# Performance work log

Measured on AMD Instinct MI355X. Metric: run time of the kernel, lower is better.

The kernel has to match this reference:

```python
import jax, jax.numpy as jnp
import numpy as np

B, D, N = 8192, 1024, 4096     # batch, input_dim, num_outputs
SEG, W_SEG = 256, 16           # 256 uniform segments of width 16 (SEG*W_SEG == N)
TAU = 0.2                      # gumbel-softmax temperature


def setup_inputs() -> dict:
    key = jax.random.key(0)
    k1, k2, k3, k4 = jax.random.split(key, 4)
    bound = 1.0 / np.sqrt(D)   # init_bounded from the original module
    x = jax.random.normal(k1, (B, D), jnp.float32)
    W = jax.random.uniform(k2, (D, N), jnp.float32, -bound, bound)
    b = jax.random.uniform(k3, (N,), jnp.float32, -bound, bound)
    # Standard Gumbel(0,1) noise, precomputed for determinism: g = -log(-log(U))
    u = jax.random.uniform(k4, (B, N), jnp.float32, 1e-10, 1.0)
    gumbel = -jnp.log(-jnp.log(u))
    # segment flags: 0 -> tanh, nonzero -> gumbel-softmax (alternating)
    flags = (jnp.arange(SEG) % 2).astype(jnp.int32)
    return {"x": x, "W": W, "b": b, "gumbel": gumbel, "flags": flags}


def reference(x, W, b, gumbel, flags):
    # Dense layer
    outputs = x @ W + b                        # [B, N]
    # Segments are uniform-width, so the per-segment slice loop collapses to a reshape.
    y = outputs.reshape(B, SEG, W_SEG)         # [B, SEG, W_SEG]
    g = gumbel.reshape(B, SEG, W_SEG)
    # gumbel-softmax over each segment (hard=False path of the original)
    soft = jax.nn.softmax((y + g) / TAU, axis=-1)
    # per-segment dispatch: flag==0 -> tanh, else gumbel-softmax
    data_t = jnp.where(flags[None, :, None] == 0, jnp.tanh(y), soft)
    return outputs, data_t.reshape(B, N)
```

## Files before the change

kernel.cpp:

```cpp
#include <hip/hip_runtime.h>
#include <hip/hip_bf16.h>

#define B_DIM 8192
#define D_DIM 1024
#define N_DIM 4096
#define TAU_INV 5.0f

typedef __bf16 bf16x8 __attribute__((ext_vector_type(8)));
typedef __bf16 bf16x4 __attribute__((ext_vector_type(4)));
typedef float  f32x4  __attribute__((ext_vector_type(4)));

__device__ __forceinline__ void gld_lds16(const void* g, void* l) {
  __builtin_amdgcn_global_load_lds((const __attribute__((address_space(1))) void*)g,
                                   (__attribute__((address_space(3))) void*)l,
                                   16, 0, 0);
}
__device__ __forceinline__ float fast_rcp(float x) {
  return __builtin_amdgcn_rcpf(x);
}
#define MFMA(a, b, c) __builtin_amdgcn_mfma_f32_16x16x32_bf16((a), (b), (c), 0, 0, 0)

__global__ void prep_x(const float* __restrict__ x, __bf16* __restrict__ xh) {
  const int i = blockIdx.x * blockDim.x + threadIdx.x;
  const int base = i * 4;
  const float4 v = *reinterpret_cast<const float4*>(x + base);
  bf16x4 h;
  h[0] = (__bf16)v.x; h[1] = (__bf16)v.y; h[2] = (__bf16)v.z; h[3] = (__bf16)v.w;
  *reinterpret_cast<bf16x4*>(xh + base) = h;
}

__global__ void prep_w(const float* __restrict__ W, __bf16* __restrict__ wht) {
  __shared__ float tile[32][33];
  const int tn = blockIdx.x & 127;
  const int tk = blockIdx.x >> 7;
  const int tx = threadIdx.x & 31;
  const int ty = threadIdx.x >> 5;
#pragma unroll
  for (int r = 0; r < 4; ++r) {
    const int k = tk * 32 + ty + r * 8;
    tile[ty + r * 8][tx] = W[(size_t)k * N_DIM + tn * 32 + tx];
  }
  __syncthreads();
#pragma unroll
  for (int r = 0; r < 4; ++r) {
    const int nn = tn * 32 + ty + r * 8;
    const int kk = tk * 32 + tx;
    wht[(size_t)nn * D_DIM + kk] = (__bf16)tile[tx][ty + r * 8];
  }
}

#define BM 128
#define BN 256
#define BK 32
#define THREADS 512

__global__ __launch_bounds__(THREADS, 4) void gemm_fused(
    const __bf16* __restrict__ xh,
    const __bf16* __restrict__ wht,
    const float* __restrict__ bias, const float* __restrict__ gumbel,
    const int* __restrict__ flags, float* __restrict__ out) {
  __shared__ __align__(16) __bf16 As[2][BM * BK];
  __shared__ __align__(16) __bf16 Bs[2][BN * BK];
  float* Ebuf = reinterpret_cast<float*>(&Bs[0][0]);

  const int tid  = threadIdx.x;
  const int lane = tid & 63;
  const int wave = tid >> 6;
  const int wr   = wave >> 2;
  const int wc   = wave & 3;
  const int fr   = lane & 15;
  const int q4   = lane >> 4;
  const int prot8 = ((q4 + ((fr >> 1) & 3)) & 3) * 8;

  const int bx  = blockIdx.x;
  const int xcd = bx & 7;
  const int ii  = bx >> 3;
  const int tn  = ii >> 3;
  const int tm  = xcd * 8 + (ii & 7);
  const int row0 = tm * BM;
  const int col0 = tn * BN;

  const int r0 = tid >> 2;
  const int l8 = (((tid & 3) - ((tid >> 3) & 3)) & 3) * 8;

  const __bf16* Ahi = xh  + (size_t)row0 * D_DIM;
  const __bf16* Bsc = wht + (size_t)col0 * D_DIM;

#define STAGE(b, t_)                                                         \
  do {                                                                       \
    const int ko_ = (t_) * 32;                                               \
    gld_lds16(Ahi + (size_t)r0 * D_DIM + ko_ + l8, &As[b][tid * 8]);         \
    gld_lds16(Bsc + (size_t)r0 * D_DIM + ko_ + l8, &Bs[b][tid * 8]);         \
    gld_lds16(Bsc + (size_t)(128 + r0) * D_DIM + ko_ + l8,                   \
              &Bs[b][(512 + tid) * 8]);                                      \
  } while (0)

#define COMPUTE(b)                                                           \
  {                                                                          \
    bf16x8 bfr_[4];                                                          \
    _Pragma("unroll")                                                        \
    for (int n = 0; n < 4; ++n)                                              \
      bfr_[n] = *reinterpret_cast<const bf16x8*>(                            \
          &Bs[b][(wc * 64 + n * 16 + fr) * BK + prot8]);                     \
    __builtin_amdgcn_s_setprio(1);                                           \
    _Pragma("unroll")                                                        \
    for (int m = 0; m < 4; ++m) {                                            \
      const bf16x8 av_ = *reinterpret_cast<const bf16x8*>(                   \
          &As[b][(wr * 64 + m * 16 + fr) * BK + prot8]);                     \
      _Pragma("unroll")                                                      \
      for (int n = 0; n < 4; ++n)                                            \
        acc[m][n] = MFMA(bfr_[n], av_, acc[m][n]);                           \
    }                                                                        \
    __builtin_amdgcn_s_setprio(0);                                           \
  }

#define VM3 asm volatile("s_waitcnt vmcnt(3)" ::: "memory")
#define VM0 asm volatile("s_waitcnt vmcnt(0)" ::: "memory")
#define BAR __builtin_amdgcn_s_barrier()

  f32x4 acc[4][4];
#pragma unroll
  for (int m = 0; m < 4; ++m)
#pragma unroll
    for (int n = 0; n < 4; ++n) acc[m][n] = (f32x4){0.f, 0.f, 0.f, 0.f};

  STAGE(0, 0);
#pragma unroll 1
  for (int it = 0; it < 15; ++it) {
    STAGE(1, 2 * it + 1);
    VM3; BAR;
    COMPUTE(0)
    BAR;
    STAGE(0, 2 * it + 2);
    VM3; BAR;
    COMPUTE(1)
    BAR;
  }
  STAGE(1, 31);
  VM3; BAR;
  COMPUTE(0)
  BAR;
  VM0; BAR;
  COMPUTE(1)

  float* out0 = out;
  float* out1 = out + (size_t)B_DIM * N_DIM;

  const int tcol = tid & 63;
  const int gcol = col0 + tcol * 4;
  const float4 bias4 = *reinterpret_cast<const float4*>(bias + gcol);
  const int flag = flags[(col0 >> 4) + (tcol >> 2)];

#pragma unroll
  for (int ck = 0; ck < 4; ++ck) {
    __syncthreads();
    if (wr == (ck >> 1)) {
#pragma unroll
      for (int mi = 0; mi < 2; ++mi) {
        const int lrow = mi * 16 + fr;
        const int m = (ck & 1) * 2 + mi;
#pragma unroll
        for (int n = 0; n < 4; ++n) {
          const int s = (wc * 16 + n * 4 + q4) ^ (lrow & 7);
          *reinterpret_cast<f32x4*>(&Ebuf[lrow * 256 + s * 4]) = acc[m][n];
        }
      }
    }
    __syncthreads();
#pragma unroll
    for (int rr = 0; rr < 4; ++rr) {
      const int lrow = rr * 8 + wave;
      const int grow = row0 + ck * 32 + lrow;
      const f32x4 a = *reinterpret_cast<const f32x4*>(
          &Ebuf[lrow * 256 + (tcol ^ (lrow & 7)) * 4]);
      const size_t idx = (size_t)grow * N_DIM + gcol;
      const float o0 = a[0] + bias4.x;
      const float o1 = a[1] + bias4.y;
      const float o2 = a[2] + bias4.z;
      const float o3 = a[3] + bias4.w;
      f32x4 ov = {o0, o1, o2, o3};
      __builtin_nontemporal_store(ov, reinterpret_cast<f32x4*>(out0 + idx));

      f32x4 v;
      if (flag == 0) {
        const float c0 = fminf(fmaxf(o0, -15.f), 15.f);
        const float c1 = fminf(fmaxf(o1, -15.f), 15.f);
        const float c2 = fminf(fmaxf(o2, -15.f), 15.f);
        const float c3 = fminf(fmaxf(o3, -15.f), 15.f);
        const float e0 = __expf(2.f * c0), e1 = __expf(2.f * c1);
        const float e2 = __expf(2.f * c2), e3 = __expf(2.f * c3);
        v[0] = (e0 - 1.f) * fast_rcp(e0 + 1.f);
        v[1] = (e1 - 1.f) * fast_rcp(e1 + 1.f);
        v[2] = (e2 - 1.f) * fast_rcp(e2 + 1.f);
        v[3] = (e3 - 1.f) * fast_rcp(e3 + 1.f);
      } else {
        const f32x4 g = __builtin_nontemporal_load(
            reinterpret_cast<const f32x4*>(gumbel + idx));
        const float t0 = (o0 + g[0]) * TAU_INV;
        const float t1 = (o1 + g[1]) * TAU_INV;
        const float t2 = (o2 + g[2]) * TAU_INV;
        const float t3 = (o3 + g[3]) * TAU_INV;
        float mx = fmaxf(fmaxf(t0, t1), fmaxf(t2, t3));
        mx = fmaxf(mx, __shfl_xor(mx, 1));
        mx = fmaxf(mx, __shfl_xor(mx, 2));
        const float e0 = __expf(t0 - mx), e1 = __expf(t1 - mx);
        const float e2 = __expf(t2 - mx), e3 = __expf(t3 - mx);
        float s = (e0 + e1) + (e2 + e3);
        s += __shfl_xor(s, 1);
        s += __shfl_xor(s, 2);
        const float inv = fast_rcp(s);
        v[0] = e0 * inv; v[1] = e1 * inv; v[2] = e2 * inv; v[3] = e3 * inv;
      }
      __builtin_nontemporal_store(v, reinterpret_cast<f32x4*>(out1 + idx));
    }
  }
}

__global__ void fallback_kernel(const float* __restrict__ x, const float* __restrict__ W,
                                const float* __restrict__ bias, const float* __restrict__ gumbel,
                                const int* __restrict__ flags, float* __restrict__ out) {
  const size_t idx = (size_t)blockIdx.x * blockDim.x + threadIdx.x;
  const int row = (int)(idx / N_DIM);
  const int col = (int)(idx % N_DIM);
  float o = bias[col];
  const float* xr = x + (size_t)row * D_DIM;
  for (int k = 0; k < D_DIM; ++k) o += xr[k] * W[(size_t)k * N_DIM + col];
  out[idx] = o;
  float v;
  if (flags[col >> 4] == 0) {
    const float oc = fminf(fmaxf(o, -15.f), 15.f);
    const float e2 = __expf(2.f * oc);
    v = (e2 - 1.f) / (e2 + 1.f);
  } else {
    const float t = (o + gumbel[idx]) * TAU_INV;
    float mx = t;
    mx = fmaxf(mx, __shfl_xor(mx, 1));
    mx = fmaxf(mx, __shfl_xor(mx, 2));
    mx = fmaxf(mx, __shfl_xor(mx, 4));
    mx = fmaxf(mx, __shfl_xor(mx, 8));
    float e = __expf(t - mx);
    float ssum = e;
    ssum += __shfl_xor(ssum, 1);
    ssum += __shfl_xor(ssum, 2);
    ssum += __shfl_xor(ssum, 4);
    ssum += __shfl_xor(ssum, 8);
    v = e / ssum;
  }
  out[(size_t)B_DIM * N_DIM + idx] = v;
}

extern "C" void kernel_launch(void* const* d_in, const int* in_sizes, int n_in,
                              void* d_out, int out_size, void* d_ws, size_t ws_size,
                              hipStream_t stream) {
  const float* x      = (const float*)d_in[0];
  const float* W      = (const float*)d_in[1];
  const float* bias   = (const float*)d_in[2];
  const float* gumbel = (const float*)d_in[3];
  const int*   flags  = (const int*)d_in[4];
  float* out = (float*)d_out;

  const size_t xcnt = (size_t)B_DIM * D_DIM;
  const size_t wcnt = (size_t)N_DIM * D_DIM;
  const size_t need = (xcnt + wcnt) * sizeof(__bf16);

  if (ws_size < need) {
    const long long nblocks = (long long)B_DIM * N_DIM / 256;
    fallback_kernel<<<(int)nblocks, 256, 0, stream>>>(x, W, bias, gumbel, flags, out);
    return;
  }

  __bf16* xh  = (__bf16*)d_ws;
  __bf16* wht = xh + xcnt;

  prep_x<<<xcnt / 4 / 256, 256, 0, stream>>>(x, xh);
  prep_w<<<(N_DIM / 32) * (D_DIM / 32), 256, 0, stream>>>(W, wht);
  gemm_fused<<<(B_DIM / BM) * (N_DIM / BN), THREADS, 0, stream>>>(
      xh, wht, bias, gumbel, flags, out);
}
```

Before: 155.9 us.

## Fuse x fp32-to-bf16 conversion into GEMM A-tile loading, drop prep_x kernel

Removes the separate prep_x kernel and instead has the GEMM load fp32 x rows into registers, convert them to bf16, and write them to LDS. This saves one kernel launch and a full round-trip of the bf16 copy of x through memory. In exchange, the A operand no longer uses direct global-to-LDS loads. Each x element is now read as fp32 by every column tile (16 tiles), which doubles A traffic from L2/HBM. The explicit vmcnt pipelining is replaced by __syncthreads, which may serialize loads with compute.

Measured after the change: 154.8 us. Within noise of the previous version (-0.7%).

```diff
diff --git a/kernel.cpp b/kernel.cpp
--- a/kernel.cpp
+++ b/kernel.cpp
@@ -19,15 +19,6 @@
   return __builtin_amdgcn_rcpf(x);
 }
 #define MFMA(a, b, c) __builtin_amdgcn_mfma_f32_16x16x32_bf16((a), (b), (c), 0, 0, 0)
-
-__global__ void prep_x(const float* __restrict__ x, __bf16* __restrict__ xh) {
-  const int i = blockIdx.x * blockDim.x + threadIdx.x;
-  const int base = i * 4;
-  const float4 v = *reinterpret_cast<const float4*>(x + base);
-  bf16x4 h;
-  h[0] = (__bf16)v.x; h[1] = (__bf16)v.y; h[2] = (__bf16)v.z; h[3] = (__bf16)v.w;
-  *reinterpret_cast<bf16x4*>(xh + base) = h;
-}
 
 __global__ void prep_w(const float* __restrict__ W, __bf16* __restrict__ wht) {
   __shared__ float tile[32][33];
@@ -55,7 +46,7 @@
 #define THREADS 512
 
 __global__ __launch_bounds__(THREADS, 4) void gemm_fused(
-    const __bf16* __restrict__ xh,
+    const float* __restrict__ x,
     const __bf16* __restrict__ wht,
     const float* __restrict__ bias, const float* __restrict__ gumbel,
     const int* __restrict__ flags, float* __restrict__ out) {
@@ -83,13 +74,31 @@
   const int r0 = tid >> 2;
   const int l8 = (((tid & 3) - ((tid >> 3) & 3)) & 3) * 8;
 
-  const __bf16* Ahi = xh  + (size_t)row0 * D_DIM;
+  const float*  Axf = x   + (size_t)row0 * D_DIM;
   const __bf16* Bsc = wht + (size_t)col0 * D_DIM;
 
-#define STAGE(b, t_)                                                         \
+  f32x4 a0_, a1_;
+
+#define ALOAD(t_)                                                            \
+  do {                                                                       \
+    const size_t o_ = (size_t)r0 * D_DIM + (t_) * 32 + l8;                   \
+    a0_ = *reinterpret_cast<const f32x4*>(Axf + o_);                         \
+    a1_ = *reinterpret_cast<const f32x4*>(Axf + o_ + 4);                     \
+  } while (0)
+
+#define CVTW(b)                                                              \
+  do {                                                                       \
+    bf16x8 h_;                                                               \
+    h_[0] = (__bf16)a0_[0]; h_[1] = (__bf16)a0_[1];                          \
+    h_[2] = (__bf16)a0_[2]; h_[3] = (__bf16)a0_[3];                          \
+    h_[4] = (__bf16)a1_[0]; h_[5] = (__bf16)a1_[1];                          \
+    h_[6] = (__bf16)a1_[2]; h_[7] = (__bf16)a1_[3];                          \
+    *reinterpret_cast<bf16x8*>(&As[b][tid * 8]) = h_;                        \
+  } while (0)
+
+#define BGLD(b, t_)                                                          \
   do {                                                                       \
     const int ko_ = (t_) * 32;                                               \
-    gld_lds16(Ahi + (size_t)r0 * D_DIM + ko_ + l8, &As[b][tid * 8]);         \
     gld_lds16(Bsc + (size_t)r0 * D_DIM + ko_ + l8, &Bs[b][tid * 8]);         \
     gld_lds16(Bsc + (size_t)(128 + r0) * D_DIM + ko_ + l8,                   \
               &Bs[b][(512 + tid) * 8]);                                      \
@@ -114,33 +123,32 @@
     __builtin_amdgcn_s_setprio(0);                                           \
   }
 
-#define VM3 asm volatile("s_waitcnt vmcnt(3)" ::: "memory")
-#define VM0 asm volatile("s_waitcnt vmcnt(0)" ::: "memory")
-#define BAR __builtin_amdgcn_s_barrier()
-
   f32x4 acc[4][4];
 #pragma unroll
   for (int m = 0; m < 4; ++m)
 #pragma unroll
     for (int n = 0; n < 4; ++n) acc[m][n] = (f32x4){0.f, 0.f, 0.f, 0.f};
 
-  STAGE(0, 0);
+  ALOAD(0);
+  BGLD(0, 0);
+  CVTW(0);
+  __syncthreads();
+
 #pragma unroll 1
   for (int it = 0; it < 15; ++it) {
-    STAGE(1, 2 * it + 1);
-    VM3; BAR;
+    ALOAD(2 * it + 1); BGLD(1, 2 * it + 1);
     COMPUTE(0)
-    BAR;
-    STAGE(0, 2 * it + 2);
-    VM3; BAR;
+    CVTW(1);
+    __syncthreads();
+    ALOAD(2 * it + 2); BGLD(0, 2 * it + 2);
     COMPUTE(1)
-    BAR;
-  }
-  STAGE(1, 31);
-  VM3; BAR;
+    CVTW(0);
+    __syncthreads();
+  }
+  ALOAD(31); BGLD(1, 31);
   COMPUTE(0)
-  BAR;
-  VM0; BAR;
+  CVTW(1);
+  __syncthreads();
   COMPUTE(1)
 
   float* out0 = out;
@@ -259,9 +267,8 @@
   const int*   flags  = (const int*)d_in[4];
   float* out = (float*)d_out;
 
-  const size_t xcnt = (size_t)B_DIM * D_DIM;
   const size_t wcnt = (size_t)N_DIM * D_DIM;
-  const size_t need = (xcnt + wcnt) * sizeof(__bf16);
+  const size_t need = wcnt * sizeof(__bf16);
 
   if (ws_size < need) {
     const long long nblocks = (long long)B_DIM * N_DIM / 256;
@@ -269,11 +276,9 @@
     return;
   }
 
-  __bf16* xh  = (__bf16*)d_ws;
-  __bf16* wht = xh + xcnt;
-
-  prep_x<<<xcnt / 4 / 256, 256, 0, stream>>>(x, xh);
+  __bf16* wht = (__bf16*)d_ws;
+
   prep_w<<<(N_DIM / 32) * (D_DIM / 32), 256, 0, stream>>>(W, wht);
   gemm_fused<<<(B_DIM / BM) * (N_DIM / BN), THREADS, 0, stream>>>(
-      xh, wht, bias, gumbel, flags, out);
-}
+      x, wht, bias, gumbel, flags, out);
+}
```

## Load A fragments directly into registers, keep only B in LDS

Applied to the files above, without the earlier changes.

Removes the LDS staging buffer for the A (activation) tile and has each wave load its A MFMA fragments straight from global memory into double-buffered registers. B is still staged through LDS via global_load_lds. The aim is to cut LDS traffic and LDS footprint for A. In exchange, A rows are re-read from global/L2 by every column wave, register pressure rises, and the fine-grained vmcnt waits are replaced by full __syncthreads, which may reduce overlap of loads with MFMA work.

Result: slower. 231.8 us (+48.7%).

```diff
diff --git a/kernel.cpp b/kernel.cpp
--- a/kernel.cpp
+++ b/kernel.cpp
@@ -59,7 +59,6 @@
     const __bf16* __restrict__ wht,
     const float* __restrict__ bias, const float* __restrict__ gumbel,
     const int* __restrict__ flags, float* __restrict__ out) {
-  __shared__ __align__(16) __bf16 As[2][BM * BK];
   __shared__ __align__(16) __bf16 Bs[2][BN * BK];
   float* Ebuf = reinterpret_cast<float*>(&Bs[0][0]);
 
@@ -70,6 +69,7 @@
   const int wc   = wave & 3;
   const int fr   = lane & 15;
   const int q4   = lane >> 4;
+  const int ko   = q4 * 8;
   const int prot8 = ((q4 + ((fr >> 1) & 3)) & 3) * 8;
 
   const int bx  = blockIdx.x;
@@ -83,19 +83,28 @@
   const int r0 = tid >> 2;
   const int l8 = (((tid & 3) - ((tid >> 3) & 3)) & 3) * 8;
 
-  const __bf16* Ahi = xh  + (size_t)row0 * D_DIM;
   const __bf16* Bsc = wht + (size_t)col0 * D_DIM;
-
-#define STAGE(b, t_)                                                         \
+  const __bf16* Afr = xh + (size_t)(row0 + wr * 64 + fr) * D_DIM + ko;
+
+  bf16x8 af0[4], af1[4];
+
+#define ALD(dst, t_)                                                         \
+  do {                                                                       \
+    _Pragma("unroll")                                                        \
+    for (int m = 0; m < 4; ++m)                                              \
+      dst[m] = *reinterpret_cast<const bf16x8*>(                             \
+          Afr + (size_t)(m * 16) * D_DIM + (t_) * 32);                       \
+  } while (0)
+
+#define BGLD(b, t_)                                                          \
   do {                                                                       \
     const int ko_ = (t_) * 32;                                               \
-    gld_lds16(Ahi + (size_t)r0 * D_DIM + ko_ + l8, &As[b][tid * 8]);         \
     gld_lds16(Bsc + (size_t)r0 * D_DIM + ko_ + l8, &Bs[b][tid * 8]);         \
     gld_lds16(Bsc + (size_t)(128 + r0) * D_DIM + ko_ + l8,                   \
               &Bs[b][(512 + tid) * 8]);                                      \
   } while (0)
 
-#define COMPUTE(b)                                                           \
+#define COMPUTE(b, af)                                                       \
   {                                                                          \
     bf16x8 bfr_[4];                                                          \
     _Pragma("unroll")                                                        \
@@ -105,43 +114,36 @@
     __builtin_amdgcn_s_setprio(1);                                           \
     _Pragma("unroll")                                                        \
     for (int m = 0; m < 4; ++m) {                                            \
-      const bf16x8 av_ = *reinterpret_cast<const bf16x8*>(                   \
-          &As[b][(wr * 64 + m * 16 + fr) * BK + prot8]);                     \
       _Pragma("unroll")                                                      \
       for (int n = 0; n < 4; ++n)                                            \
-        acc[m][n] = MFMA(bfr_[n], av_, acc[m][n]);                           \
+        acc[m][n] = MFMA(bfr_[n], af[m], acc[m][n]);                         \
     }                                                                        \
     __builtin_amdgcn_s_setprio(0);                                           \
   }
 
-#define VM3 asm volatile("s_waitcnt vmcnt(3)" ::: "memory")
-#define VM0 asm volatile("s_waitcnt vmcnt(0)" ::: "memory")
-#define BAR __builtin_amdgcn_s_barrier()
-
   f32x4 acc[4][4];
 #pragma unroll
   for (int m = 0; m < 4; ++m)
 #pragma unroll
     for (int n = 0; n < 4; ++n) acc[m][n] = (f32x4){0.f, 0.f, 0.f, 0.f};
 
-  STAGE(0, 0);
+  ALD(af0, 0);
+  BGLD(0, 0);
+  __syncthreads();
+
 #pragma unroll 1
   for (int it = 0; it < 15; ++it) {
-    STAGE(1, 2 * it + 1);
-    VM3; BAR;
-    COMPUTE(0)
-    BAR;
-    STAGE(0, 2 * it + 2);
-    VM3; BAR;
-    COMPUTE(1)
-    BAR;
-  }
-  STAGE(1, 31);
-  VM3; BAR;
-  COMPUTE(0)
-  BAR;
-  VM0; BAR;
-  COMPUTE(1)
+    ALD(af1, 2 * it + 1); BGLD(1, 2 * it + 1);
+    COMPUTE(0, af0)
+    __syncthreads();
+    ALD(af0, 2 * it + 2); BGLD(0, 2 * it + 2);
+    COMPUTE(1, af1)
+    __syncthreads();
+  }
+  ALD(af1, 31); BGLD(1, 31);
+  COMPUTE(0, af0)
+  __syncthreads();
+  COMPUTE(1, af1)
 
   float* out0 = out;
   float* out1 = out + (size_t)B_DIM * N_DIM;
```
